# Kernel tuning notes

Hardware: AMD Instinct MI355X
Metric: run time of the kernel (lower is better)

Reference implementation:

```python
import jax, jax.numpy as jnp
import numpy as np

H, W = 1024, 2048      # dims from __init__
C = 34                 # Cityscapes label ids 0..33 (thing classes 24..33)
N_INST = 128           # instance capacity (len(instance_probs))


def setup_inputs() -> dict:
    key = jax.random.key(0)
    k1, k2, k3, k4 = jax.random.split(key, 4)
    return {
        "segmentation_map": jax.random.randint(k1, (H, W), 0, C, dtype=jnp.int32),
        "instance_maps": jax.random.randint(k2, (H, W), 0, N_INST + 1, dtype=jnp.int32),
        "seg_map_probs": jax.random.uniform(k3, (C, H, W), dtype=jnp.float32),
        "instance_probs": jax.random.uniform(k4, (N_INST,), dtype=jnp.float32),
    }


def reference(segmentation_map, instance_maps, seg_map_probs, instance_probs):
    # nn.Threshold(23.99, 50): x if x > 23.99 else 50; then things = (thresh <= 33)
    seg_f = segmentation_map.astype(jnp.float32)
    things = (seg_f > 23.99) & (seg_f <= 33.0)           # (H, W) bool
    inst = jnp.where(things, instance_maps, 0)            # zero-out non-thing pixels

    flat_inst = inst.reshape(-1)                          # (HW,)
    flat_seg = segmentation_map.reshape(-1)               # (HW,)

    # segmented histogram: pixel counts per (instance, class)
    pair_idx = flat_inst * C + flat_seg
    counts2d = jax.ops.segment_sum(
        jnp.ones_like(flat_inst), pair_idx, num_segments=(N_INST + 1) * C
    ).reshape(N_INST + 1, C)

    # segmented sum of every class prob map over each instance mask
    probs_pix = seg_map_probs.reshape(C, -1).T            # (HW, C)
    sums2d = jax.ops.segment_sum(probs_pix, flat_inst, num_segments=N_INST + 1)  # (N+1, C)

    counts = counts2d[1:]                                 # drop background id 0 -> (N, C)
    sums = sums2d[1:]                                     # (N, C)

    inst_class = jnp.argmax(counts, axis=1).astype(jnp.int32)     # mode class per instance
    total = counts.sum(axis=1)                                     # seg_counts.sum()
    # mean of the winning class's prob map over the instance mask
    seg_prob = jnp.take_along_axis(sums, inst_class[:, None], axis=1)[:, 0] / jnp.maximum(
        total, 1
    ).astype(seg_map_probs.dtype)

    # per-instance binary masks, uint8 like the torch code
    inst_ids = jnp.arange(1, N_INST + 1, dtype=inst.dtype)
    inst_masks = (inst[None, :, :] == inst_ids[:, None, None]).astype(jnp.uint8)  # (N, H, W)

    valid = total > 0   # which instance slots actually appear in the image
    return inst_masks, inst_class, instance_probs, seg_prob, total, valid
```

## Files before the change

kernel.cpp:

```cpp
#include <hip/hip_runtime.h>

#define HH   1024
#define WW   2048
#define HWP  (HH * WW)
#define CC   34
#define NI   128
#define THING_LO 24
#define THING_HI 33
#define NTC  10

#define CHUNK 8192
#define QPB   (CHUNK / 4)

typedef float nfloat4 __attribute__((ext_vector_type(4)));

#define OFF_CLASS  ((size_t)NI * HWP)
#define OFF_PROBS  (OFF_CLASS + NI)
#define OFF_SEGP   (OFF_PROBS + NI)
#define OFF_TOTAL  (OFF_SEGP + NI)
#define OFF_VALID  (OFF_TOTAL + NI)

#define WS_COUNTS  0
#define WS_CLS     (NI * NTC * 4)
#define WS_INV     (WS_CLS + NI * 4)

__device__ __forceinline__ int thing_inst(int s, int im) {
    return (s >= THING_LO && s <= THING_HI) ? im : 0;
}

__global__ __launch_bounds__(256) void k1_mask_count(
    const int* __restrict__ seg, const int* __restrict__ imap,
    float* __restrict__ out_masks, int* __restrict__ counts)
{
    __shared__ uint32_t inst4[QPB];
    __shared__ int      hist[NI * NTC];

    const int tid = threadIdx.x;

    for (int i = tid; i < NI * NTC; i += 256) hist[i] = 0;
    __syncthreads();

    const int base_q = blockIdx.x * QPB;
    #pragma unroll
    for (int j = 0; j < QPB / 256; ++j) {
        const int q = base_q + j * 256 + tid;
        const int p = q * 4;
        const int4 sg = *reinterpret_cast<const int4*>(seg + p);
        const int4 im = *reinterpret_cast<const int4*>(imap + p);

        const int i0 = thing_inst(sg.x, im.x);
        const int i1 = thing_inst(sg.y, im.y);
        const int i2 = thing_inst(sg.z, im.z);
        const int i3 = thing_inst(sg.w, im.w);

        if (i0 > 0) atomicAdd(&hist[(i0 - 1) * NTC + (sg.x - THING_LO)], 1);
        if (i1 > 0) atomicAdd(&hist[(i1 - 1) * NTC + (sg.y - THING_LO)], 1);
        if (i2 > 0) atomicAdd(&hist[(i2 - 1) * NTC + (sg.z - THING_LO)], 1);
        if (i3 > 0) atomicAdd(&hist[(i3 - 1) * NTC + (sg.w - THING_LO)], 1);

        inst4[j * 256 + tid] = (uint32_t)i0 | ((uint32_t)i1 << 8) |
                               ((uint32_t)i2 << 16) | ((uint32_t)i3 << 24);
    }
    __syncthreads();

    for (int i = tid; i < NI * NTC; i += 256) {
        const int v = hist[i];
        if (v) atomicAdd(&counts[i], v);
    }

    const int w = tid >> 6;
    const int l = tid & 63;
    float* obase = out_masks + (size_t)blockIdx.x * CHUNK + (size_t)(l * 4);

    for (int ip = 0; ip < 32; ++ip) {
        const uint32_t id = (uint32_t)(w * 32 + ip + 1);
        float* o = obase + (size_t)(w * 32 + ip) * HWP;
        #pragma unroll 8
        for (int s = 0; s < 32; ++s) {
            const uint32_t qq = inst4[s * 64 + l];
            nfloat4 v;
            v.x = ((qq & 0xffu)         == id) ? 1.0f : 0.0f;
            v.y = (((qq >> 8)  & 0xffu) == id) ? 1.0f : 0.0f;
            v.z = (((qq >> 16) & 0xffu) == id) ? 1.0f : 0.0f;
            v.w = ((qq >> 24)           == id) ? 1.0f : 0.0f;
            *reinterpret_cast<nfloat4*>(o + s * 256) = v;
        }
    }
}

__global__ __launch_bounds__(128) void k2_stats(
    const int* __restrict__ counts, const float* __restrict__ iprobs,
    float* __restrict__ out, int* __restrict__ cls_ws, float* __restrict__ inv_ws)
{
    const int i = threadIdx.x;
    int bestv = 0, bestc = 0, tot = 0;
    #pragma unroll
    for (int j = 0; j < NTC; ++j) {
        const int c = counts[i * NTC + j];
        tot += c;
        if (c > bestv) { bestv = c; bestc = THING_LO + j; }
    }
    cls_ws[i] = bestc;
    inv_ws[i] = 1.0f / (float)(tot > 0 ? tot : 1);
    out[OFF_CLASS + i] = (float)bestc;
    out[OFF_PROBS + i] = iprobs[i];
    out[OFF_SEGP  + i] = 0.0f;
    out[OFF_TOTAL + i] = (float)tot;
    out[OFF_VALID + i] = (tot > 0) ? 1.0f : 0.0f;
}

__global__ __launch_bounds__(256) void k3_segsum(
    const int* __restrict__ seg, const int* __restrict__ imap,
    const float* __restrict__ probs, const int* __restrict__ cls_ws,
    const float* __restrict__ inv_ws, float* __restrict__ out)
{
    __shared__ float lsum[NI];
    __shared__ int   scls[NI];
    if (threadIdx.x < NI) {
        lsum[threadIdx.x] = 0.0f;
        scls[threadIdx.x] = cls_ws[threadIdx.x];
    }
    __syncthreads();

    const int stride = gridDim.x * blockDim.x;
    for (int t = blockIdx.x * blockDim.x + threadIdx.x; t < HWP / 4; t += stride) {
        const int p = t * 4;
        const int4 sg = *reinterpret_cast<const int4*>(seg + p);
        const int4 im = *reinterpret_cast<const int4*>(imap + p);
        const int ii[4] = { thing_inst(sg.x, im.x), thing_inst(sg.y, im.y),
                            thing_inst(sg.z, im.z), thing_inst(sg.w, im.w) };
        #pragma unroll
        for (int k = 0; k < 4; ++k) {
            if (ii[k] > 0) {
                const int inst = ii[k] - 1;
                const size_t idx = (size_t)scls[inst] * HWP + (size_t)(p + k);
                atomicAdd(&lsum[inst], probs[idx]);
            }
        }
    }
    __syncthreads();
    if (threadIdx.x < NI) {
        const float v = lsum[threadIdx.x];
        if (v != 0.0f)
            atomicAdd(&out[OFF_SEGP + threadIdx.x], v * inv_ws[threadIdx.x]);
    }
}

extern "C" void kernel_launch(void* const* d_in, const int* in_sizes, int n_in,
                              void* d_out, int out_size, void* d_ws, size_t ws_size,
                              hipStream_t stream) {
    const int*   seg    = (const int*)d_in[0];
    const int*   imap   = (const int*)d_in[1];
    const float* probs  = (const float*)d_in[2];
    const float* iprobs = (const float*)d_in[3];
    float* out = (float*)d_out;

    char* ws = (char*)d_ws;
    int*   counts = (int*)(ws + WS_COUNTS);
    int*   cls_ws = (int*)(ws + WS_CLS);
    float* inv_ws = (float*)(ws + WS_INV);

    (void)hipMemsetAsync(counts, 0, NI * NTC * sizeof(int), stream);

    k1_mask_count<<<HWP / CHUNK, 256, 0, stream>>>(seg, imap, out, counts);
    k2_stats<<<1, 128, 0, stream>>>(counts, iprobs, out, cls_ws, inv_ws);
    k3_segsum<<<1024, 256, 0, stream>>>(seg, imap, probs, cls_ws, inv_ws, out);
}
```

Measured before the change: 1.213 ms.

## Split mask kernel: stage packed instance ids in workspace, plane-major mask writes

The fused mask/count kernel is split in two. The first kernel computes the packed 8-bit instance ids and the histogram and stores the packed ids in a global workspace. The second kernel writes each mask plane contiguously from that workspace, giving each block one plane chunk so stores are long and sequential instead of strided across 128 planes. The segment-sum kernel now reads the packed ids (4 bytes per 4 pixels instead of 32) and skips words with no thing pixels. The cost is an extra launch and an 8 MB workspace round trip.

```diff
diff --git a/kernel.cpp b/kernel.cpp
--- a/kernel.cpp
+++ b/kernel.cpp
@@ -9,8 +9,14 @@
 #define THING_HI 33
 #define NTC  10
 
-#define CHUNK 8192
-#define QPB   (CHUNK / 4)
+#define NW   (HWP / 4)
+
+#define K1A_BLOCKS 256
+#define K1A_WPT    8
+
+#define NCHUNK  16
+#define CWORDS  (NW / NCHUNK)
+#define CPIX    (HWP / NCHUNK)
 
 typedef float nfloat4 __attribute__((ext_vector_type(4)));
 
@@ -23,27 +29,25 @@
 #define WS_COUNTS  0
 #define WS_CLS     (NI * NTC * 4)
 #define WS_INV     (WS_CLS + NI * 4)
+#define WS_INST    8192
 
 __device__ __forceinline__ int thing_inst(int s, int im) {
     return (s >= THING_LO && s <= THING_HI) ? im : 0;
 }
 
-__global__ __launch_bounds__(256) void k1_mask_count(
+__global__ __launch_bounds__(256) void k1a_inst(
     const int* __restrict__ seg, const int* __restrict__ imap,
-    float* __restrict__ out_masks, int* __restrict__ counts)
+    uint32_t* __restrict__ instw, int* __restrict__ counts)
 {
-    __shared__ uint32_t inst4[QPB];
-    __shared__ int      hist[NI * NTC];
-
+    __shared__ int hist[NI * NTC];
     const int tid = threadIdx.x;
-
     for (int i = tid; i < NI * NTC; i += 256) hist[i] = 0;
     __syncthreads();
 
-    const int base_q = blockIdx.x * QPB;
+    const int base = blockIdx.x * (K1A_WPT * 256);
     #pragma unroll
-    for (int j = 0; j < QPB / 256; ++j) {
-        const int q = base_q + j * 256 + tid;
+    for (int j = 0; j < K1A_WPT; ++j) {
+        const int q = base + j * 256 + tid;
         const int p = q * 4;
         const int4 sg = *reinterpret_cast<const int4*>(seg + p);
         const int4 im = *reinterpret_cast<const int4*>(imap + p);
@@ -58,8 +62,8 @@
         if (i2 > 0) atomicAdd(&hist[(i2 - 1) * NTC + (sg.z - THING_LO)], 1);
         if (i3 > 0) atomicAdd(&hist[(i3 - 1) * NTC + (sg.w - THING_LO)], 1);
 
-        inst4[j * 256 + tid] = (uint32_t)i0 | ((uint32_t)i1 << 8) |
-                               ((uint32_t)i2 << 16) | ((uint32_t)i3 << 24);
+        instw[q] = (uint32_t)i0 | ((uint32_t)i1 << 8) |
+                   ((uint32_t)i2 << 16) | ((uint32_t)i3 << 24);
     }
     __syncthreads();
 
@@ -67,24 +71,28 @@
         const int v = hist[i];
         if (v) atomicAdd(&counts[i], v);
     }
+}
 
-    const int w = tid >> 6;
-    const int l = tid & 63;
-    float* obase = out_masks + (size_t)blockIdx.x * CHUNK + (size_t)(l * 4);
+__global__ __launch_bounds__(256) void k1b_masks(
+    const uint32_t* __restrict__ instw, float* __restrict__ out_masks)
+{
+    const int plane = blockIdx.x & (NI - 1);
+    const int chunk = blockIdx.x >> 7;
+    const uint32_t id = (uint32_t)(plane + 1);
 
-    for (int ip = 0; ip < 32; ++ip) {
-        const uint32_t id = (uint32_t)(w * 32 + ip + 1);
-        float* o = obase + (size_t)(w * 32 + ip) * HWP;
-        #pragma unroll 8
-        for (int s = 0; s < 32; ++s) {
-            const uint32_t qq = inst4[s * 64 + l];
-            nfloat4 v;
-            v.x = ((qq & 0xffu)         == id) ? 1.0f : 0.0f;
-            v.y = (((qq >> 8)  & 0xffu) == id) ? 1.0f : 0.0f;
-            v.z = (((qq >> 16) & 0xffu) == id) ? 1.0f : 0.0f;
-            v.w = ((qq >> 24)           == id) ? 1.0f : 0.0f;
-            *reinterpret_cast<nfloat4*>(o + s * 256) = v;
-        }
+    const uint32_t* src = instw + (size_t)chunk * CWORDS;
+    float* dst = out_masks + (size_t)plane * HWP + (size_t)chunk * CPIX;
+    const int tid = threadIdx.x;
+
+    #pragma unroll 4
+    for (int i = 0; i < CWORDS / 256; ++i) {
+        const uint32_t qq = src[i * 256 + tid];
+        nfloat4 v;
+        v.x = ((qq & 0xffu)         == id) ? 1.0f : 0.0f;
+        v.y = (((qq >> 8)  & 0xffu) == id) ? 1.0f : 0.0f;
+        v.z = (((qq >> 16) & 0xffu) == id) ? 1.0f : 0.0f;
+        v.w = ((qq >> 24)           == id) ? 1.0f : 0.0f;
+        *reinterpret_cast<nfloat4*>(dst + (size_t)(i * 256 + tid) * 4) = v;
     }
 }
 
@@ -110,9 +118,9 @@
 }
 
 __global__ __launch_bounds__(256) void k3_segsum(
-    const int* __restrict__ seg, const int* __restrict__ imap,
-    const float* __restrict__ probs, const int* __restrict__ cls_ws,
-    const float* __restrict__ inv_ws, float* __restrict__ out)
+    const uint32_t* __restrict__ instw, const float* __restrict__ probs,
+    const int* __restrict__ cls_ws, const float* __restrict__ inv_ws,
+    float* __restrict__ out)
 {
     __shared__ float lsum[NI];
     __shared__ int   scls[NI];
@@ -123,18 +131,17 @@
     __syncthreads();
 
     const int stride = gridDim.x * blockDim.x;
-    for (int t = blockIdx.x * blockDim.x + threadIdx.x; t < HWP / 4; t += stride) {
-        const int p = t * 4;
-        const int4 sg = *reinterpret_cast<const int4*>(seg + p);
-        const int4 im = *reinterpret_cast<const int4*>(imap + p);
-        const int ii[4] = { thing_inst(sg.x, im.x), thing_inst(sg.y, im.y),
-                            thing_inst(sg.z, im.z), thing_inst(sg.w, im.w) };
-        #pragma unroll
-        for (int k = 0; k < 4; ++k) {
-            if (ii[k] > 0) {
-                const int inst = ii[k] - 1;
-                const size_t idx = (size_t)scls[inst] * HWP + (size_t)(p + k);
-                atomicAdd(&lsum[inst], probs[idx]);
+    for (int q = blockIdx.x * blockDim.x + threadIdx.x; q < NW; q += stride) {
+        const uint32_t wv = instw[q];
+        if (wv) {
+            const int p = q * 4;
+            #pragma unroll
+            for (int k = 0; k < 4; ++k) {
+                const int inst = (int)((wv >> (8 * k)) & 0xffu);
+                if (inst) {
+                    const size_t idx = (size_t)scls[inst - 1] * HWP + (size_t)(p + k);
+                    atomicAdd(&lsum[inst - 1], probs[idx]);
+                }
             }
         }
     }
@@ -156,13 +163,15 @@
     float* out = (float*)d_out;
 
     char* ws = (char*)d_ws;
-    int*   counts = (int*)(ws + WS_COUNTS);
-    int*   cls_ws = (int*)(ws + WS_CLS);
-    float* inv_ws = (float*)(ws + WS_INV);
+    int*      counts = (int*)(ws + WS_COUNTS);
+    int*      cls_ws = (int*)(ws + WS_CLS);
+    float*    inv_ws = (float*)(ws + WS_INV);
+    uint32_t* instw  = (uint32_t*)(ws + WS_INST);
 
     (void)hipMemsetAsync(counts, 0, NI * NTC * sizeof(int), stream);
 
-    k1_mask_count<<<HWP / CHUNK, 256, 0, stream>>>(seg, imap, out, counts);
-    k2_stats<<<1, 128, 0, stream>>>(counts, iprobs, out, cls_ws, inv_ws);
-    k3_segsum<<<1024, 256, 0, stream>>>(seg, imap, probs, cls_ws, inv_ws, out);
+    k1a_inst <<<K1A_BLOCKS, 256, 0, stream>>>(seg, imap, instw, counts);
+    k2_stats <<<1, 128, 0, stream>>>(counts, iprobs, out, cls_ws, inv_ws);
+    k1b_masks<<<NI * NCHUNK, 256, 0, stream>>>(instw, out);
+    k3_segsum<<<1024, 256, 0, stream>>>(instw, probs, cls_ws, inv_ws, out);
 }
```

Result: no change. 1.211 ms (-0.1%).
